# Performance work log

Measured on AMD Instinct MI355X. Metric: run time of the kernel, lower is better.

## Reference

```python
import jax, jax.numpy as jnp
import numpy as np

B, S, D, E = 4, 4096, 1024, 8


def setup_inputs() -> dict:
    key = jax.random.key(0)
    ks = jax.random.split(key, 6)
    x = jax.random.normal(ks[0], (B, S, D), dtype=jnp.float32)
    router_mask = jax.random.randint(ks[1], (B, S), 0, 2)
    We = jax.random.normal(ks[2], (E, D, D), dtype=jnp.float32) * (1.0 / np.sqrt(D))
    be = jax.random.normal(ks[3], (E, D), dtype=jnp.float32) * 0.02
    Wg = jax.random.normal(ks[4], (D, E), dtype=jnp.float32) * (1.0 / np.sqrt(D))
    bg = jax.random.normal(ks[5], (E,), dtype=jnp.float32) * 0.02
    return {"x": x, "router_mask": router_mask, "We": We, "be": be,
            "Wg": Wg, "bg": bg, "top_k": 2}


def reference(x, router_mask, We, be, Wg, bg, top_k):
    # Gating: raw logits (the original uses top-k LOGITS as combine weights,
    # with no softmax). router_mask is accepted but unused, as in the source.
    gate_logits = jnp.einsum('bsd,de->bse', x, Wg) + bg            # [B,S,E]
    top_logits, top_idx = jax.lax.top_k(gate_logits, top_k)        # [B,S,K]
    # Dense all-expert outputs, then gather the selected ones per token.
    expert_out = jnp.einsum('bsd,edf->bsef', x, We) + be           # [B,S,E,D]
    sel = jnp.take_along_axis(expert_out, top_idx[..., None], axis=2)  # [B,S,K,D]
    out = jnp.sum(sel * top_logits[..., None], axis=2)             # [B,S,D]
    return out
```

## Files before the change

### kernel.cpp

```cpp
#include <hip/hip_runtime.h>


#define TOK 16384
#define DIM 1024
#define NE 8
#define NPAIR 28

typedef __attribute__((ext_vector_type(8))) short bf16x8;
typedef __attribute__((ext_vector_type(4))) float f32x4;

#define OFF_CNT    0u
#define OFF_FLAG   132u
#define OFF_TOKW   1024u
#define OFF_PLIST  132096u
#define OFF_WT     1049600u
#define OFF_XB     17826816u
#define OFF_PIDX   51381248u
#define NEED_T3    1049600u
#define NEED_T2    17826816u
#define NEED_T1    51397632u

__device__ __forceinline__ float bf2f(unsigned short u) {
  union { unsigned int i; float f; } c; c.i = ((unsigned int)u) << 16; return c.f;
}
__device__ __forceinline__ unsigned short f2bf_rne(float f) {
  union { float f; unsigned int i; } c; c.f = f;
  unsigned int i = c.i + 0x7fffu + ((c.i >> 16) & 1u);
  return (unsigned short)(i >> 16);
}
__device__ __forceinline__ unsigned int pk2(float lo, float hi) {
  union { float f; unsigned int i; } a, b; a.f = lo; b.f = hi;
  return ((b.i + 0x8000u) & 0xFFFF0000u) | ((a.i + 0x8000u) >> 16);
}

typedef const __attribute__((address_space(1))) unsigned int gas_uint;
typedef __attribute__((address_space(3))) unsigned int las_uint;
__device__ __forceinline__ void gl_lds16(const void* g, void* l) {
  __builtin_amdgcn_global_load_lds((gas_uint*)g, (las_uint*)l, 16, 0, 0);
}
__device__ __forceinline__ void drain_vm() {
  asm volatile("s_waitcnt vmcnt(0)" ::: "memory");
}

__global__ void init_detect(const unsigned int* __restrict__ xdw,
                            int* __restrict__ cnt, int* __restrict__ flag) {
  __shared__ int h;
  if (threadIdx.x == 0) h = 0;
  __syncthreads();
  if (threadIdx.x < 32) cnt[threadIdx.x] = 0;
  unsigned int idx = (threadIdx.x * 32749u + 7u) & 0x7FFFFFu;
  unsigned int b = (xdw[idx] >> 7) & 0xFFu;
  atomicAdd(&h, (b >= 112u && b <= 132u) ? 1 : 0);
  __syncthreads();
  if (threadIdx.x == 0) flag[0] = (h >= 128) ? 1 : 0;
}

#define TP 136
__global__ __launch_bounds__(256) void transpose_W3(const void* __restrict__ Wev,
                                                    unsigned short* __restrict__ Wt,
                                                    const int* __restrict__ flag) {
  const int isbf = *flag;
  __shared__ __align__(16) unsigned short tile[128 * TP];
  const int k0 = blockIdx.x * 128, n0 = blockIdx.y * 128;
  const size_t ebase = (size_t)blockIdx.z << 20;
  const int tid = threadIdx.x;
  const int r = tid >> 1, h = tid & 1;
  if (isbf) {
    const unsigned short* s = (const unsigned short*)Wev + ebase + (size_t)(k0 + r) * DIM + n0 + h * 64;
#pragma unroll
    for (int c = 0; c < 8; ++c)
      *(uint4*)&tile[r * TP + h * 64 + c * 8] = *(const uint4*)(s + c * 8);
  } else {
    const float* s = (const float*)Wev + ebase + (size_t)(k0 + r) * DIM + n0 + h * 64;
#pragma unroll
    for (int c = 0; c < 8; ++c) {
      float4 f0 = *(const float4*)(s + c * 8);
      float4 f1 = *(const float4*)(s + c * 8 + 4);
      uint4 v;
      v.x = pk2(f0.x, f0.y); v.y = pk2(f0.z, f0.w);
      v.z = pk2(f1.x, f1.y); v.w = pk2(f1.z, f1.w);
      *(uint4*)&tile[r * TP + h * 64 + c * 8] = v;
    }
  }
  __syncthreads();
  const int kc = tid & 15;
#pragma unroll
  for (int pass = 0; pass < 8; ++pass) {
    const int nl = pass * 16 + (tid >> 4);
    unsigned short ob[8];
#pragma unroll
    for (int j = 0; j < 8; ++j) ob[j] = tile[(kc * 8 + j) * TP + nl];
    unsigned short* dst = Wt + ebase + (size_t)(n0 + nl) * DIM + k0 + kc * 8;
    *(uint4*)dst = *(uint4*)&ob[0];
  }
}

__global__ __launch_bounds__(256) void gating_v8(
    const void* __restrict__ xv, const void* __restrict__ Wgv,
    const void* __restrict__ bgv, const int* __restrict__ flag,
    unsigned char* __restrict__ pairidx, float2* __restrict__ tokw,
    unsigned short* __restrict__ xb) {
  const int isbf = *flag;
  const int tid = threadIdx.x;
  const int lane = tid & 63;
  const int t = blockIdx.x * 4 + (tid >> 6);

  __shared__ float wgT[NE][DIM];

  if (isbf) {
    const unsigned short* wg = (const unsigned short*)Wgv + (size_t)tid * 32;
#pragma unroll
    for (int rr = 0; rr < 4; ++rr) {
      union { uint4 v; unsigned short s[8]; } w;
      w.v = *(const uint4*)(wg + rr * 8);
      const int d = tid * 4 + rr;
#pragma unroll
      for (int e = 0; e < NE; ++e) wgT[e][d] = bf2f(w.s[e]);
    }
  } else {
    const float* wg = (const float*)Wgv + (size_t)tid * 32;
#pragma unroll
    for (int rr = 0; rr < 4; ++rr) {
      float4 w0 = *(const float4*)(wg + rr * 8);
      float4 w1 = *(const float4*)(wg + rr * 8 + 4);
      const int d = tid * 4 + rr;
      wgT[0][d] = w0.x; wgT[1][d] = w0.y; wgT[2][d] = w0.z; wgT[3][d] = w0.w;
      wgT[4][d] = w1.x; wgT[5][d] = w1.y; wgT[6][d] = w1.z; wgT[7][d] = w1.w;
    }
  }
  __syncthreads();

  float acc[NE];
#pragma unroll
  for (int e = 0; e < NE; ++e) acc[e] = 0.f;

  if (isbf) {
    const unsigned short* xp = (const unsigned short*)xv + (size_t)t * DIM;
#pragma unroll
    for (int j = 0; j < 8; ++j) {
      const int d = j * 128 + lane * 2;
      const unsigned int xw = *(const unsigned int*)(xp + d);
      const float x0 = bf2f((unsigned short)(xw & 0xFFFFu));
      const float x1 = bf2f((unsigned short)(xw >> 16));
#pragma unroll
      for (int e = 0; e < NE; ++e)
        acc[e] += x0 * wgT[e][d] + x1 * wgT[e][d + 1];
    }
  } else {
    const float* xp = (const float*)xv + (size_t)t * DIM;
    unsigned short* xo = xb + (size_t)t * DIM;
#pragma unroll
    for (int j = 0; j < 8; ++j) {
      const int d = j * 128 + lane * 2;
      const float2 xl = *(const float2*)(xp + d);
      *(unsigned int*)(xo + d) = pk2(xl.x, xl.y);
#pragma unroll
      for (int e = 0; e < NE; ++e)
        acc[e] += xl.x * wgT[e][d] + xl.y * wgT[e][d + 1];
    }
  }
#pragma unroll
  for (int m = 1; m < 64; m <<= 1) {
#pragma unroll
    for (int e = 0; e < NE; ++e) acc[e] += __shfl_xor(acc[e], m);
  }
  if (lane == 0) {
    if (isbf) {
      union { uint4 v; unsigned short s[8]; } bgv8; bgv8.v = *(const uint4*)bgv;
#pragma unroll
      for (int e = 0; e < NE; ++e) acc[e] += bf2f(bgv8.s[e]);
    } else {
      const float* bgp = (const float*)bgv;
#pragma unroll
      for (int e = 0; e < NE; ++e) acc[e] += bgp[e];
    }
    int e0 = 0; float v0 = acc[0];
#pragma unroll
    for (int e = 1; e < NE; ++e) if (acc[e] > v0) { v0 = acc[e]; e0 = e; }
    int e1 = -1; float v1 = -3.4e38f;
#pragma unroll
    for (int e = 0; e < NE; ++e) if (e != e0 && acc[e] > v1) { v1 = acc[e]; e1 = e; }
    const int a = e0 < e1 ? e0 : e1;
    const int b = e0 < e1 ? e1 : e0;
    const float wa = (a == e0) ? v0 : v1;
    const float wb = (a == e0) ? v1 : v0;
    const int pidx = a * 7 - (a * (a - 1)) / 2 + (b - a - 1);
    pairidx[t] = (unsigned char)pidx;
    tokw[t] = make_float2(wa, wb);
  }
}

__global__ __launch_bounds__(256) void build_plist(
    const unsigned char* __restrict__ pairidx, int* __restrict__ cnt,
    unsigned short* __restrict__ plist) {
  const int p = blockIdx.x;
  const int tid = threadIdx.x, lane = tid & 63, wv = tid >> 6;
  __shared__ int wcnt[4];
  __shared__ int sbase;
  if (tid == 0) sbase = 0;
  __syncthreads();
  const unsigned long long lanemask = (1ull << lane) - 1ull;
  for (int c = 0; c < TOK / 1024; ++c) {
    const int t0 = c * 1024 + tid * 4;
    const uchar4 pv = *(const uchar4*)(pairidx + t0);
    const unsigned long long m0 = __ballot(pv.x == (unsigned char)p);
    const unsigned long long m1 = __ballot(pv.y == (unsigned char)p);
    const unsigned long long m2 = __ballot(pv.z == (unsigned char)p);
    const unsigned long long m3 = __ballot(pv.w == (unsigned char)p);
    const int c0 = __popcll(m0), c1 = __popcll(m1);
    const int c2 = __popcll(m2), c3 = __popcll(m3);
    if (lane == 0) wcnt[wv] = c0 + c1 + c2 + c3;
    __syncthreads();
    int off = sbase;
    for (int w2 = 0; w2 < wv; ++w2) off += wcnt[w2];
    if (pv.x == (unsigned char)p) plist[p * TOK + off + __popcll(m0 & lanemask)] = (unsigned short)(t0 + 0);
    off += c0;
    if (pv.y == (unsigned char)p) plist[p * TOK + off + __popcll(m1 & lanemask)] = (unsigned short)(t0 + 1);
    off += c1;
    if (pv.z == (unsigned char)p) plist[p * TOK + off + __popcll(m2 & lanemask)] = (unsigned short)(t0 + 2);
    off += c2;
    if (pv.w == (unsigned char)p) plist[p * TOK + off + __popcll(m3 & lanemask)] = (unsigned short)(t0 + 3);
    const int tot = wcnt[0] + wcnt[1] + wcnt[2] + wcnt[3];
    __syncthreads();
    if (tid == 0) sbase += tot;
  }
  if (tid == 0) cnt[p] = sbase;
}

__global__ __launch_bounds__(256, 2) void moe_gemm_v3(
    const void* __restrict__ xv, const unsigned short* __restrict__ xb,
    const unsigned short* __restrict__ Wt, const void* __restrict__ bev,
    const int* __restrict__ flag, const int* __restrict__ cnt,
    const unsigned short* __restrict__ plist, const float2* __restrict__ tokw,
    void* __restrict__ outv) {
  const int y = blockIdx.x;
  int p = -1, mt = 0, acc8 = 0;
  for (int q = 0; q < NPAIR; ++q) {
    const int t = (cnt[q] + 127) >> 7;
    if (y < acc8 + t) { p = q; mt = y - acc8; break; }
    acc8 += t;
  }
  if (p < 0) return;
  const int count = cnt[p];
  int a = 0, rem = p;
  while (rem >= 7 - a) { rem -= 7 - a; ++a; }
  const int ea = a, eb = a + 1 + rem;
  const int isbf = *flag;
  const unsigned char* abase = isbf ? (const unsigned char*)xv
                                    : (const unsigned char*)xb;

  const int tid = threadIdx.x;
  const int lane = tid & 63;
  const int w = tid >> 6;
  const int wr = w >> 1, wc = w & 1;
  const int n0 = blockIdx.y * 128;

  __shared__ __align__(16) unsigned short Alds[128 * 64];
  __shared__ __align__(16) unsigned short Wlds[256 * 64];

  const int csrc = (lane & 7) ^ (lane >> 3);

  const unsigned char* aptr[4];
#pragma unroll
  for (int li = 0; li < 4; ++li) {
    int rg = mt * 128 + w * 32 + li * 8 + (lane >> 3);
    int rgc = rg < count ? rg : count - 1;
    int tok = (int)plist[p * TOK + rgc];
    aptr[li] = abase + (size_t)tok * (DIM * 2) + csrc * 16;
  }
  const unsigned char* wptr[8];
#pragma unroll
  for (int li = 0; li < 8; ++li) {
    int R = w * 64 + li * 8 + (lane >> 3);
    size_t e = (size_t)((R >> 7) ? eb : ea);
    int n = R & 127;
    wptr[li] = (const unsigned char*)Wt + (e << 21) + (size_t)(n0 + n) * (DIM * 2) + csrc * 16;
  }

  f32x4 accA[4][4], accB[4][4];
#pragma unroll
  for (int i = 0; i < 4; ++i)
#pragma unroll
    for (int j = 0; j < 4; ++j) { accA[i][j] = (f32x4){0,0,0,0}; accB[i][j] = (f32x4){0,0,0,0}; }

  for (int ks = 0; ks < DIM; ks += 64) {
#pragma unroll
    for (int li = 0; li < 4; ++li)
      gl_lds16(aptr[li] + ks * 2, (char*)Alds + (w * 32 + li * 8) * 128);
#pragma unroll
    for (int li = 0; li < 8; ++li)
      gl_lds16(wptr[li] + ks * 2, (char*)Wlds + (w * 64 + li * 8) * 128);
    drain_vm();
    __syncthreads();
    const int rl = lane & 15;
#pragma unroll
    for (int kst = 0; kst < 2; ++kst) {
      const int chunk = kst * 4 + (lane >> 4);
      bf16x8 af[4];
#pragma unroll
      for (int m4 = 0; m4 < 4; ++m4) {
        const int r = wr * 64 + m4 * 16 + rl;
        af[m4] = *(const bf16x8*)&Alds[r * 64 + ((chunk ^ (r & 7)) << 3)];
      }
#pragma unroll
      for (int nt = 0; nt < 4; ++nt) {
        const int n = wc * 64 + nt * 16 + rl;
        const int wo = (chunk ^ (n & 7)) << 3;
        bf16x8 bA = *(const bf16x8*)&Wlds[n * 64 + wo];
        bf16x8 bB = *(const bf16x8*)&Wlds[(128 + n) * 64 + wo];
#pragma unroll
        for (int m4 = 0; m4 < 4; ++m4) {
          accA[m4][nt] = __builtin_amdgcn_mfma_f32_16x16x32_bf16(af[m4], bA, accA[m4][nt], 0, 0, 0);
          accB[m4][nt] = __builtin_amdgcn_mfma_f32_16x16x32_bf16(af[m4], bB, accB[m4][nt], 0, 0, 0);
        }
      }
    }
    __syncthreads();
  }

  const int col_l = lane & 15, quad = lane >> 4;
  float bea[4], beb[4];
#pragma unroll
  for (int nt = 0; nt < 4; ++nt) {
    const int col = n0 + wc * 64 + nt * 16 + col_l;
    if (isbf) {
      bea[nt] = bf2f(((const unsigned short*)bev)[ea * DIM + col]);
      beb[nt] = bf2f(((const unsigned short*)bev)[eb * DIM + col]);
    } else {
      bea[nt] = ((const float*)bev)[ea * DIM + col];
      beb[nt] = ((const float*)bev)[eb * DIM + col];
    }
  }
#pragma unroll
  for (int m4 = 0; m4 < 4; ++m4) {
#pragma unroll
    for (int j = 0; j < 4; ++j) {
      const int rg = mt * 128 + wr * 64 + m4 * 16 + quad * 4 + j;
      if (rg < count) {
        const int tk = (int)plist[p * TOK + rg];
        const float2 wt2 = tokw[tk];
#pragma unroll
        for (int nt = 0; nt < 4; ++nt) {
          const float o = wt2.x * (accA[m4][nt][j] + bea[nt]) + wt2.y * (accB[m4][nt][j] + beb[nt]);
          const size_t oi = (size_t)tk * DIM + n0 + wc * 64 + nt * 16 + col_l;
          if (isbf) ((unsigned short*)outv)[oi] = f2bf_rne(o);
          else      ((float*)outv)[oi] = o;
        }
      }
    }
  }
}

__global__ __launch_bounds__(256) void gating_fb(const void* __restrict__ xv,
                                                 const void* __restrict__ Wgv,
                                                 const void* __restrict__ bgv,
                                                 const int* __restrict__ flag,
                                                 int* __restrict__ cnt,
                                                 unsigned short* __restrict__ plist,
                                                 float2* __restrict__ tokw) {
  const int isbf = *flag;
  const int lane = threadIdx.x & 63;
  const int t = blockIdx.x * 4 + (threadIdx.x >> 6);
  float acc[NE];
#pragma unroll
  for (int e = 0; e < NE; ++e) acc[e] = 0.f;
  if (isbf) {
    const unsigned short* xp = (const unsigned short*)xv + (size_t)t * DIM + lane * 16;
#pragma unroll
    for (int u = 0; u < 2; ++u) {
      union { uint4 v; unsigned short s[8]; } xr; xr.v = *(const uint4*)(xp + u * 8);
#pragma unroll
      for (int j = 0; j < 8; ++j) {
        const int d = lane * 16 + u * 8 + j;
        union { uint4 v; unsigned short s[8]; } wg;
        wg.v = *(const uint4*)((const unsigned short*)Wgv + (size_t)d * 8);
        const float xf = bf2f(xr.s[j]);
#pragma unroll
        for (int e = 0; e < NE; ++e) acc[e] += xf * bf2f(wg.s[e]);
      }
    }
  } else {
    const float* xp = (const float*)xv + (size_t)t * DIM + lane * 16;
    float xr[16];
#pragma unroll
    for (int u = 0; u < 4; ++u) *(float4*)&xr[u * 4] = *(const float4*)(xp + u * 4);
#pragma unroll
    for (int j = 0; j < 16; ++j) {
      const int d = lane * 16 + j;
      const float* wr = (const float*)Wgv + (size_t)d * 8;
      float4 w0 = *(const float4*)wr, w1 = *(const float4*)(wr + 4);
      const float xf = xr[j];
      acc[0] += xf * w0.x; acc[1] += xf * w0.y; acc[2] += xf * w0.z; acc[3] += xf * w0.w;
      acc[4] += xf * w1.x; acc[5] += xf * w1.y; acc[6] += xf * w1.z; acc[7] += xf * w1.w;
    }
  }
#pragma unroll
  for (int m = 1; m < 64; m <<= 1) {
#pragma unroll
    for (int e = 0; e < NE; ++e) acc[e] += __shfl_xor(acc[e], m);
  }
  if (lane == 0) {
    if (isbf) {
      union { uint4 v; unsigned short s[8]; } bgv8; bgv8.v = *(const uint4*)bgv;
#pragma unroll
      for (int e = 0; e < NE; ++e) acc[e] += bf2f(bgv8.s[e]);
    } else {
      const float* bgp = (const float*)bgv;
#pragma unroll
      for (int e = 0; e < NE; ++e) acc[e] += bgp[e];
    }
    int e0 = 0; float v0 = acc[0];
#pragma unroll
    for (int e = 1; e < NE; ++e) if (acc[e] > v0) { v0 = acc[e]; e0 = e; }
    int e1 = -1; float v1 = -3.4e38f;
#pragma unroll
    for (int e = 0; e < NE; ++e) if (e != e0 && acc[e] > v1) { v1 = acc[e]; e1 = e; }
    const int a = e0 < e1 ? e0 : e1;
    const int b = e0 < e1 ? e1 : e0;
    const float wa = (a == e0) ? v0 : v1;
    const float wb = (a == e0) ? v1 : v0;
    const int pidx = a * 7 - (a * (a - 1)) / 2 + (b - a - 1);
    const int pos = atomicAdd(&cnt[pidx], 1);
    plist[pidx * TOK + pos] = (unsigned short)t;
    tokw[t] = make_float2(wa, wb);
  }
}

template <int TIER>
__global__ __launch_bounds__(256, 2) void moe_gemm(
    const void* __restrict__ xv, const unsigned short* __restrict__ Wt,
    const void* __restrict__ Wev, const void* __restrict__ bev,
    const int* __restrict__ flag, const int* __restrict__ cnt,
    const unsigned short* __restrict__ plist, const float2* __restrict__ tokw,
    void* __restrict__ outv) {
  const int y = blockIdx.y;
  int p = -1, mt = 0, acc8 = 0;
  for (int q = 0; q < NPAIR; ++q) {
    const int t = (cnt[q] + 127) >> 7;
    if (y < acc8 + t) { p = q; mt = y - acc8; break; }
    acc8 += t;
  }
  if (p < 0) return;
  const int count = cnt[p];
  int a = 0, rem = p;
  while (rem >= 7 - a) { rem -= 7 - a; ++a; }
  const int ea = a, eb = a + 1 + rem;
  const int isbf = *flag;

  const int tid = threadIdx.x;
  const int lane = tid & 63;
  const int w = tid >> 6;
  const int wr = w >> 1, wc = w & 1;
  const int n0 = blockIdx.x * 128;

  __shared__ __align__(16) unsigned short Alds[128 * 64];
  __shared__ __align__(16) unsigned short Wlds[256 * 64];

  const int csrc = (lane & 7) ^ (lane >> 3);

  const char* aptr[4];
#pragma unroll
  for (int li = 0; li < 4; ++li) {
    int rg = mt * 128 + w * 32 + li * 8 + (lane >> 3);
    int rgc = rg < count ? rg : count - 1;
    int tok = (int)plist[p * TOK + rgc];
    aptr[li] = (const char*)xv + (size_t)tok * (DIM * 2) + csrc * 16;
  }
  const char* wptr[8];
#pragma unroll
  for (int li = 0; li < 8; ++li) {
    int R = w * 64 + li * 8 + (lane >> 3);
    size_t e = (size_t)((R >> 7) ? eb : ea);
    int n = R & 127;
    wptr[li] = (const char*)Wt + (e << 21) + (size_t)(n0 + n) * (DIM * 2) + csrc * 16;
  }
  const int rF = tid >> 1;
  const float* xrowF = nullptr;
  if (!isbf) {
    int rg = mt * 128 + rF;
    int rgc = rg < count ? rg : count - 1;
    xrowF = (const float*)xv + (size_t)plist[p * TOK + rgc] * DIM;
  }

  f32x4 accA[4][4], accB[4][4];
#pragma unroll
  for (int i = 0; i < 4; ++i)
#pragma unroll
    for (int j = 0; j < 4; ++j) { accA[i][j] = (f32x4){0,0,0,0}; accB[i][j] = (f32x4){0,0,0,0}; }

  for (int ks = 0; ks < DIM; ks += 64) {
    if (isbf) {
#pragma unroll
      for (int li = 0; li < 4; ++li)
        gl_lds16(aptr[li] + ks * 2, (char*)Alds + (w * 32 + li * 8) * 128);
    } else {
#pragma unroll
      for (int i = 0; i < 4; ++i) {
        const int cst = (tid & 1) * 4 + i;
        const int cs = cst ^ (rF & 7);
        const float* s = xrowF + ks + cs * 8;
        float4 f0 = *(const float4*)s, f1 = *(const float4*)(s + 4);
        uint4 v;
        v.x = pk2(f0.x, f0.y); v.y = pk2(f0.z, f0.w);
        v.z = pk2(f1.x, f1.y); v.w = pk2(f1.z, f1.w);
        *(uint4*)&Alds[rF * 64 + cst * 8] = v;
      }
    }
    if (TIER == 2) {
#pragma unroll
      for (int li = 0; li < 8; ++li)
        gl_lds16(wptr[li] + ks * 2, (char*)Wlds + (w * 64 + li * 8) * 128);
    } else {
      const int kk = tid >> 2, noff = (tid & 3) * 32;
#pragma unroll
      for (int h = 0; h < 2; ++h) {
        const size_t eb2 = (size_t)(h ? eb : ea) << 20;
        unsigned short wb[32];
        if (isbf) {
          const unsigned short* s = (const unsigned short*)Wev + eb2 + (size_t)(ks + kk) * DIM + n0 + noff;
#pragma unroll
          for (int jj = 0; jj < 4; ++jj) *(uint4*)&wb[jj * 8] = *(const uint4*)(s + jj * 8);
        } else {
          const float* s = (const float*)Wev + eb2 + (size_t)(ks + kk) * DIM + n0 + noff;
#pragma unroll
          for (int jj = 0; jj < 8; ++jj) {
            float4 f = *(const float4*)(s + jj * 4);
            unsigned int lo = pk2(f.x, f.y), hi = pk2(f.z, f.w);
            wb[jj * 4 + 0] = (unsigned short)(lo & 0xFFFF);
            wb[jj * 4 + 1] = (unsigned short)(lo >> 16);
            wb[jj * 4 + 2] = (unsigned short)(hi & 0xFFFF);
            wb[jj * 4 + 3] = (unsigned short)(hi >> 16);
          }
        }
        const int chunk = kk >> 3, kin = kk & 7;
#pragma unroll
        for (int j = 0; j < 32; ++j) {
          const int n = noff + j;
          Wlds[(h * 128 + n) * 64 + ((chunk ^ (n & 7)) << 3) + kin] = wb[j];
        }
      }
    }
    __syncthreads();
    const int rl = lane & 15;
#pragma unroll
    for (int kst = 0; kst < 2; ++kst) {
      const int chunk = kst * 4 + (lane >> 4);
      bf16x8 af[4];
#pragma unroll
      for (int m4 = 0; m4 < 4; ++m4) {
        const int r = wr * 64 + m4 * 16 + rl;
        af[m4] = *(const bf16x8*)&Alds[r * 64 + ((chunk ^ (r & 7)) << 3)];
      }
#pragma unroll
      for (int nt = 0; nt < 4; ++nt) {
        const int n = wc * 64 + nt * 16 + rl;
        const int wo = (chunk ^ (n & 7)) << 3;
        bf16x8 bA = *(const bf16x8*)&Wlds[n * 64 + wo];
        bf16x8 bB = *(const bf16x8*)&Wlds[(128 + n) * 64 + wo];
#pragma unroll
        for (int m4 = 0; m4 < 4; ++m4) {
          accA[m4][nt] = __builtin_amdgcn_mfma_f32_16x16x32_bf16(af[m4], bA, accA[m4][nt], 0, 0, 0);
          accB[m4][nt] = __builtin_amdgcn_mfma_f32_16x16x32_bf16(af[m4], bB, accB[m4][nt], 0, 0, 0);
        }
      }
    }
    __syncthreads();
  }

  const int col_l = lane & 15, quad = lane >> 4;
  float bea[4], beb[4];
#pragma unroll
  for (int nt = 0; nt < 4; ++nt) {
    const int col = n0 + wc * 64 + nt * 16 + col_l;
    if (isbf) {
      bea[nt] = bf2f(((const unsigned short*)bev)[ea * DIM + col]);
      beb[nt] = bf2f(((const unsigned short*)bev)[eb * DIM + col]);
    } else {
      bea[nt] = ((const float*)bev)[ea * DIM + col];
      beb[nt] = ((const float*)bev)[eb * DIM + col];
    }
  }
#pragma unroll
  for (int m4 = 0; m4 < 4; ++m4) {
#pragma unroll
    for (int j = 0; j < 4; ++j) {
      const int rg = mt * 128 + wr * 64 + m4 * 16 + quad * 4 + j;
      if (rg < count) {
        const int tk = (int)plist[p * TOK + rg];
        const float2 wt2 = tokw[tk];
#pragma unroll
        for (int nt = 0; nt < 4; ++nt) {
          const float o = wt2.x * (accA[m4][nt][j] + bea[nt]) + wt2.y * (accB[m4][nt][j] + beb[nt]);
          const size_t oi = (size_t)tk * DIM + n0 + wc * 64 + nt * 16 + col_l;
          if (isbf) ((unsigned short*)outv)[oi] = f2bf_rne(o);
          else      ((float*)outv)[oi] = o;
        }
      }
    }
  }
}

extern "C" void kernel_launch(void* const* d_in, const int* in_sizes, int n_in,
                              void* d_out, int out_size, void* d_ws, size_t ws_size,
                              hipStream_t stream) {
  const void* xv  = d_in[0];
  const void* Wev = d_in[2];
  const void* bev = d_in[3];
  const void* Wgv = d_in[4];
  const void* bgv = d_in[5];

  char* ws = (char*)d_ws;
  int* cnt    = (int*)(ws + OFF_CNT);
  int* flag   = (int*)(ws + OFF_FLAG);
  float2* tokw = (float2*)(ws + OFF_TOKW);
  unsigned short* plist = (unsigned short*)(ws + OFF_PLIST);
  unsigned short* Wt    = (unsigned short*)(ws + OFF_WT);

  if (ws_size < (size_t)NEED_T3) return;
  const int tier = (ws_size >= (size_t)NEED_T1) ? 1
                 : (ws_size >= (size_t)NEED_T2) ? 2 : 3;

  init_detect<<<1, 256, 0, stream>>>((const unsigned int*)xv, cnt, flag);
  if (tier <= 2) transpose_W3<<<dim3(8, 8, 8), 256, 0, stream>>>(Wev, Wt, flag);

  if (tier == 1) {
    unsigned short* xb = (unsigned short*)(ws + OFF_XB);
    unsigned char* pairidx = (unsigned char*)(ws + OFF_PIDX);
    gating_v8<<<TOK / 4, 256, 0, stream>>>(xv, Wgv, bgv, flag, pairidx, tokw, xb);
    build_plist<<<NPAIR, 256, 0, stream>>>(pairidx, cnt, plist);
    moe_gemm_v3<<<dim3(160, 8), 256, 0, stream>>>(xv, xb, Wt, bev, flag, cnt,
                                                  plist, tokw, d_out);
  } else if (tier == 2) {
    gating_fb<<<TOK / 4, 256, 0, stream>>>(xv, Wgv, bgv, flag, cnt, plist, tokw);
    moe_gemm<2><<<dim3(8, 160), 256, 0, stream>>>(xv, Wt, Wev, bev, flag, cnt,
                                                  plist, tokw, d_out);
  } else {
    gating_fb<<<TOK / 4, 256, 0, stream>>>(xv, Wgv, bgv, flag, cnt, plist, tokw);
    moe_gemm<3><<<dim3(8, 160), 256, 0, stream>>>(xv, Wt, Wev, bev, flag, cnt,
                                                  plist, tokw, d_out);
  }
}
```

Before: 285.4 us.

## Fuse weight transpose with gating and detect dtype on host

The weight-transpose blocks and the gating blocks now run in one templated prep kernel, dispatched by block index, so the two stages can overlap and one launch goes away. The input dtype is read from the host-side input size, which removes the init_detect launch and the runtime flag branches in the GEMM (new moe_gemm_v4 template). The old low-workspace fallback tiers are dropped, so the code now returns early when the workspace is too small. It relies on build_plist to write the counts, since they are no longer zeroed first.

Result: no change. 282.4 us (-1.1%).

```diff
diff --git a/kernel.cpp b/kernel.cpp
--- a/kernel.cpp
+++ b/kernel.cpp
@@ -42,72 +42,60 @@
   asm volatile("s_waitcnt vmcnt(0)" ::: "memory");
 }
 
-__global__ void init_detect(const unsigned int* __restrict__ xdw,
-                            int* __restrict__ cnt, int* __restrict__ flag) {
-  __shared__ int h;
-  if (threadIdx.x == 0) h = 0;
-  __syncthreads();
-  if (threadIdx.x < 32) cnt[threadIdx.x] = 0;
-  unsigned int idx = (threadIdx.x * 32749u + 7u) & 0x7FFFFFu;
-  unsigned int b = (xdw[idx] >> 7) & 0xFFu;
-  atomicAdd(&h, (b >= 112u && b <= 132u) ? 1 : 0);
-  __syncthreads();
-  if (threadIdx.x == 0) flag[0] = (h >= 128) ? 1 : 0;
-}
-
 #define TP 136
-__global__ __launch_bounds__(256) void transpose_W3(const void* __restrict__ Wev,
-                                                    unsigned short* __restrict__ Wt,
-                                                    const int* __restrict__ flag) {
-  const int isbf = *flag;
-  __shared__ __align__(16) unsigned short tile[128 * TP];
-  const int k0 = blockIdx.x * 128, n0 = blockIdx.y * 128;
-  const size_t ebase = (size_t)blockIdx.z << 20;
+
+
+template <int ISBF>
+__global__ __launch_bounds__(256) void prep(
+    const void* __restrict__ xv, const void* __restrict__ Wgv,
+    const void* __restrict__ bgv, const void* __restrict__ Wev,
+    unsigned short* __restrict__ Wt, unsigned char* __restrict__ pairidx,
+    float2* __restrict__ tokw, unsigned short* __restrict__ xb) {
+  __shared__ __align__(16) char smem[128 * TP * 2];
   const int tid = threadIdx.x;
-  const int r = tid >> 1, h = tid & 1;
-  if (isbf) {
-    const unsigned short* s = (const unsigned short*)Wev + ebase + (size_t)(k0 + r) * DIM + n0 + h * 64;
-#pragma unroll
-    for (int c = 0; c < 8; ++c)
-      *(uint4*)&tile[r * TP + h * 64 + c * 8] = *(const uint4*)(s + c * 8);
-  } else {
-    const float* s = (const float*)Wev + ebase + (size_t)(k0 + r) * DIM + n0 + h * 64;
-#pragma unroll
-    for (int c = 0; c < 8; ++c) {
-      float4 f0 = *(const float4*)(s + c * 8);
-      float4 f1 = *(const float4*)(s + c * 8 + 4);
-      uint4 v;
-      v.x = pk2(f0.x, f0.y); v.y = pk2(f0.z, f0.w);
-      v.z = pk2(f1.x, f1.y); v.w = pk2(f1.z, f1.w);
-      *(uint4*)&tile[r * TP + h * 64 + c * 8] = v;
-    }
-  }
-  __syncthreads();
-  const int kc = tid & 15;
-#pragma unroll
-  for (int pass = 0; pass < 8; ++pass) {
-    const int nl = pass * 16 + (tid >> 4);
-    unsigned short ob[8];
-#pragma unroll
-    for (int j = 0; j < 8; ++j) ob[j] = tile[(kc * 8 + j) * TP + nl];
-    unsigned short* dst = Wt + ebase + (size_t)(n0 + nl) * DIM + k0 + kc * 8;
-    *(uint4*)dst = *(uint4*)&ob[0];
-  }
-}
-
-__global__ __launch_bounds__(256) void gating_v8(
-    const void* __restrict__ xv, const void* __restrict__ Wgv,
-    const void* __restrict__ bgv, const int* __restrict__ flag,
-    unsigned char* __restrict__ pairidx, float2* __restrict__ tokw,
-    unsigned short* __restrict__ xb) {
-  const int isbf = *flag;
-  const int tid = threadIdx.x;
+
+  if (blockIdx.x >= 4096) {
+    unsigned short* tile = (unsigned short*)smem;
+    const int idx = blockIdx.x - 4096;
+    const int k0 = (idx & 7) * 128, n0 = ((idx >> 3) & 7) * 128;
+    const size_t ebase = (size_t)(idx >> 6) << 20;
+    const int r = tid >> 1, h = tid & 1;
+    if (ISBF) {
+      const unsigned short* s = (const unsigned short*)Wev + ebase + (size_t)(k0 + r) * DIM + n0 + h * 64;
+#pragma unroll
+      for (int c = 0; c < 8; ++c)
+        *(uint4*)&tile[r * TP + h * 64 + c * 8] = *(const uint4*)(s + c * 8);
+    } else {
+      const float* s = (const float*)Wev + ebase + (size_t)(k0 + r) * DIM + n0 + h * 64;
+#pragma unroll
+      for (int c = 0; c < 8; ++c) {
+        float4 f0 = *(const float4*)(s + c * 8);
+        float4 f1 = *(const float4*)(s + c * 8 + 4);
+        uint4 v;
+        v.x = pk2(f0.x, f0.y); v.y = pk2(f0.z, f0.w);
+        v.z = pk2(f1.x, f1.y); v.w = pk2(f1.z, f1.w);
+        *(uint4*)&tile[r * TP + h * 64 + c * 8] = v;
+      }
+    }
+    __syncthreads();
+    const int kc = tid & 15;
+#pragma unroll
+    for (int pass = 0; pass < 8; ++pass) {
+      const int nl = pass * 16 + (tid >> 4);
+      unsigned short ob[8];
+#pragma unroll
+      for (int j = 0; j < 8; ++j) ob[j] = tile[(kc * 8 + j) * TP + nl];
+      unsigned short* dst = Wt + ebase + (size_t)(n0 + nl) * DIM + k0 + kc * 8;
+      *(uint4*)dst = *(uint4*)&ob[0];
+    }
+    return;
+  }
+
+  float (*wgT)[DIM] = (float(*)[DIM])smem;
   const int lane = tid & 63;
   const int t = blockIdx.x * 4 + (tid >> 6);
 
-  __shared__ float wgT[NE][DIM];
-
-  if (isbf) {
+  if (ISBF) {
     const unsigned short* wg = (const unsigned short*)Wgv + (size_t)tid * 32;
 #pragma unroll
     for (int rr = 0; rr < 4; ++rr) {
@@ -134,7 +122,7 @@
 #pragma unroll
   for (int e = 0; e < NE; ++e) acc[e] = 0.f;
 
-  if (isbf) {
+  if (ISBF) {
     const unsigned short* xp = (const unsigned short*)xv + (size_t)t * DIM;
 #pragma unroll
     for (int j = 0; j < 8; ++j) {
@@ -165,7 +153,7 @@
     for (int e = 0; e < NE; ++e) acc[e] += __shfl_xor(acc[e], m);
   }
   if (lane == 0) {
-    if (isbf) {
+    if (ISBF) {
       union { uint4 v; unsigned short s[8]; } bgv8; bgv8.v = *(const uint4*)bgv;
 #pragma unroll
       for (int e = 0; e < NE; ++e) acc[e] += bf2f(bgv8.s[e]);
@@ -227,6 +215,273 @@
   if (tid == 0) cnt[p] = sbase;
 }
 
+template <int ISBF>
+__global__ __launch_bounds__(256, 2) void moe_gemm_v4(
+    const void* __restrict__ xv, const unsigned short* __restrict__ xb,
+    const unsigned short* __restrict__ Wt, const void* __restrict__ bev,
+    const int* __restrict__ cnt, const unsigned short* __restrict__ plist,
+    const float2* __restrict__ tokw, void* __restrict__ outv) {
+  const int y = blockIdx.x;
+  int p = -1, mt = 0, acc8 = 0;
+  for (int q = 0; q < NPAIR; ++q) {
+    const int t = (cnt[q] + 127) >> 7;
+    if (y < acc8 + t) { p = q; mt = y - acc8; break; }
+    acc8 += t;
+  }
+  if (p < 0) return;
+  const int count = cnt[p];
+  int a = 0, rem = p;
+  while (rem >= 7 - a) { rem -= 7 - a; ++a; }
+  const int ea = a, eb = a + 1 + rem;
+  const unsigned char* abase = ISBF ? (const unsigned char*)xv
+                                    : (const unsigned char*)xb;
+
+  const int tid = threadIdx.x;
+  const int lane = tid & 63;
+  const int w = tid >> 6;
+  const int wr = w >> 1, wc = w & 1;
+  const int n0 = blockIdx.y * 128;
+
+  __shared__ __align__(16) unsigned short Alds[128 * 64];
+  __shared__ __align__(16) unsigned short Wlds[256 * 64];
+
+  const int csrc = (lane & 7) ^ (lane >> 3);
+
+  const unsigned char* aptr[4];
+#pragma unroll
+  for (int li = 0; li < 4; ++li) {
+    int rg = mt * 128 + w * 32 + li * 8 + (lane >> 3);
+    int rgc = rg < count ? rg : count - 1;
+    int tok = (int)plist[p * TOK + rgc];
+    aptr[li] = abase + (size_t)tok * (DIM * 2) + csrc * 16;
+  }
+  const unsigned char* wptr[8];
+#pragma unroll
+  for (int li = 0; li < 8; ++li) {
+    int R = w * 64 + li * 8 + (lane >> 3);
+    size_t e = (size_t)((R >> 7) ? eb : ea);
+    int n = R & 127;
+    wptr[li] = (const unsigned char*)Wt + (e << 21) + (size_t)(n0 + n) * (DIM * 2) + csrc * 16;
+  }
+
+  f32x4 accA[4][4], accB[4][4];
+#pragma unroll
+  for (int i = 0; i < 4; ++i)
+#pragma unroll
+    for (int j = 0; j < 4; ++j) { accA[i][j] = (f32x4){0,0,0,0}; accB[i][j] = (f32x4){0,0,0,0}; }
+
+  for (int ks = 0; ks < DIM; ks += 64) {
+#pragma unroll
+    for (int li = 0; li < 4; ++li)
+      gl_lds16(aptr[li] + ks * 2, (char*)Alds + (w * 32 + li * 8) * 128);
+#pragma unroll
+    for (int li = 0; li < 8; ++li)
+      gl_lds16(wptr[li] + ks * 2, (char*)Wlds + (w * 64 + li * 8) * 128);
+    drain_vm();
+    __syncthreads();
+    const int rl = lane & 15;
+#pragma unroll
+    for (int kst = 0; kst < 2; ++kst) {
+      const int chunk = kst * 4 + (lane >> 4);
+      bf16x8 af[4];
+#pragma unroll
+      for (int m4 = 0; m4 < 4; ++m4) {
+        const int r = wr * 64 + m4 * 16 + rl;
+        af[m4] = *(const bf16x8*)&Alds[r * 64 + ((chunk ^ (r & 7)) << 3)];
+      }
+#pragma unroll
+      for (int nt = 0; nt < 4; ++nt) {
+        const int n = wc * 64 + nt * 16 + rl;
+        const int wo = (chunk ^ (n & 7)) << 3;
+        bf16x8 bA = *(const bf16x8*)&Wlds[n * 64 + wo];
+        bf16x8 bB = *(const bf16x8*)&Wlds[(128 + n) * 64 + wo];
+#pragma unroll
+        for (int m4 = 0; m4 < 4; ++m4) {
+          accA[m4][nt] = __builtin_amdgcn_mfma_f32_16x16x32_bf16(af[m4], bA, accA[m4][nt], 0, 0, 0);
+          accB[m4][nt] = __builtin_amdgcn_mfma_f32_16x16x32_bf16(af[m4], bB, accB[m4][nt], 0, 0, 0);
+        }
+      }
+    }
+    __syncthreads();
+  }
+
+  const int col_l = lane & 15, quad = lane >> 4;
+  float bea[4], beb[4];
+#pragma unroll
+  for (int nt = 0; nt < 4; ++nt) {
+    const int col = n0 + wc * 64 + nt * 16 + col_l;
+    if (ISBF) {
+      bea[nt] = bf2f(((const unsigned short*)bev)[ea * DIM + col]);
+      beb[nt] = bf2f(((const unsigned short*)bev)[eb * DIM + col]);
+    } else {
+      bea[nt] = ((const float*)bev)[ea * DIM + col];
+      beb[nt] = ((const float*)bev)[eb * DIM + col];
+    }
+  }
+#pragma unroll
+  for (int m4 = 0; m4 < 4; ++m4) {
+#pragma unroll
+    for (int j = 0; j < 4; ++j) {
+      const int rg = mt * 128 + wr * 64 + m4 * 16 + quad * 4 + j;
+      if (rg < count) {
+        const int tk = (int)plist[p * TOK + rg];
+        const float2 wt2 = tokw[tk];
+#pragma unroll
+        for (int nt = 0; nt < 4; ++nt) {
+          const float o = wt2.x * (accA[m4][nt][j] + bea[nt]) + wt2.y * (accB[m4][nt][j] + beb[nt]);
+          const size_t oi = (size_t)tk * DIM + n0 + wc * 64 + nt * 16 + col_l;
+          if (ISBF) ((unsigned short*)outv)[oi] = f2bf_rne(o);
+          else      ((float*)outv)[oi] = o;
+        }
+      }
+    }
+  }
+}
+
+
+__global__ void init_detect(const unsigned int* __restrict__ xdw,
+                            int* __restrict__ cnt, int* __restrict__ flag) {
+  __shared__ int h;
+  if (threadIdx.x == 0) h = 0;
+  __syncthreads();
+  if (threadIdx.x < 32) cnt[threadIdx.x] = 0;
+  unsigned int idx = (threadIdx.x * 32749u + 7u) & 0x7FFFFFu;
+  unsigned int b = (xdw[idx] >> 7) & 0xFFu;
+  atomicAdd(&h, (b >= 112u && b <= 132u) ? 1 : 0);
+  __syncthreads();
+  if (threadIdx.x == 0) flag[0] = (h >= 128) ? 1 : 0;
+}
+
+__global__ __launch_bounds__(256) void transpose_W3(const void* __restrict__ Wev,
+                                                    unsigned short* __restrict__ Wt,
+                                                    const int* __restrict__ flag) {
+  const int isbf = *flag;
+  __shared__ __align__(16) unsigned short tile[128 * TP];
+  const int k0 = blockIdx.x * 128, n0 = blockIdx.y * 128;
+  const size_t ebase = (size_t)blockIdx.z << 20;
+  const int tid = threadIdx.x;
+  const int r = tid >> 1, h = tid & 1;
+  if (isbf) {
+    const unsigned short* s = (const unsigned short*)Wev + ebase + (size_t)(k0 + r) * DIM + n0 + h * 64;
+#pragma unroll
+    for (int c = 0; c < 8; ++c)
+      *(uint4*)&tile[r * TP + h * 64 + c * 8] = *(const uint4*)(s + c * 8);
+  } else {
+    const float* s = (const float*)Wev + ebase + (size_t)(k0 + r) * DIM + n0 + h * 64;
+#pragma unroll
+    for (int c = 0; c < 8; ++c) {
+      float4 f0 = *(const float4*)(s + c * 8);
+      float4 f1 = *(const float4*)(s + c * 8 + 4);
+      uint4 v;
+      v.x = pk2(f0.x, f0.y); v.y = pk2(f0.z, f0.w);
+      v.z = pk2(f1.x, f1.y); v.w = pk2(f1.z, f1.w);
+      *(uint4*)&tile[r * TP + h * 64 + c * 8] = v;
+    }
+  }
+  __syncthreads();
+  const int kc = tid & 15;
+#pragma unroll
+  for (int pass = 0; pass < 8; ++pass) {
+    const int nl = pass * 16 + (tid >> 4);
+    unsigned short ob[8];
+#pragma unroll
+    for (int j = 0; j < 8; ++j) ob[j] = tile[(kc * 8 + j) * TP + nl];
+    unsigned short* dst = Wt + ebase + (size_t)(n0 + nl) * DIM + k0 + kc * 8;
+    *(uint4*)dst = *(uint4*)&ob[0];
+  }
+}
+
+__global__ __launch_bounds__(256) void gating_v8(
+    const void* __restrict__ xv, const void* __restrict__ Wgv,
+    const void* __restrict__ bgv, const int* __restrict__ flag,
+    unsigned char* __restrict__ pairidx, float2* __restrict__ tokw,
+    unsigned short* __restrict__ xb) {
+  const int isbf = *flag;
+  const int tid = threadIdx.x;
+  const int lane = tid & 63;
+  const int t = blockIdx.x * 4 + (tid >> 6);
+  __shared__ float wgT[NE][DIM];
+  if (isbf) {
+    const unsigned short* wg = (const unsigned short*)Wgv + (size_t)tid * 32;
+#pragma unroll
+    for (int rr = 0; rr < 4; ++rr) {
+      union { uint4 v; unsigned short s[8]; } w;
+      w.v = *(const uint4*)(wg + rr * 8);
+      const int d = tid * 4 + rr;
+#pragma unroll
+      for (int e = 0; e < NE; ++e) wgT[e][d] = bf2f(w.s[e]);
+    }
+  } else {
+    const float* wg = (const float*)Wgv + (size_t)tid * 32;
+#pragma unroll
+    for (int rr = 0; rr < 4; ++rr) {
+      float4 w0 = *(const float4*)(wg + rr * 8);
+      float4 w1 = *(const float4*)(wg + rr * 8 + 4);
+      const int d = tid * 4 + rr;
+      wgT[0][d] = w0.x; wgT[1][d] = w0.y; wgT[2][d] = w0.z; wgT[3][d] = w0.w;
+      wgT[4][d] = w1.x; wgT[5][d] = w1.y; wgT[6][d] = w1.z; wgT[7][d] = w1.w;
+    }
+  }
+  __syncthreads();
+  float acc[NE];
+#pragma unroll
+  for (int e = 0; e < NE; ++e) acc[e] = 0.f;
+  if (isbf) {
+    const unsigned short* xp = (const unsigned short*)xv + (size_t)t * DIM;
+#pragma unroll
+    for (int j = 0; j < 8; ++j) {
+      const int d = j * 128 + lane * 2;
+      const unsigned int xw = *(const unsigned int*)(xp + d);
+      const float x0 = bf2f((unsigned short)(xw & 0xFFFFu));
+      const float x1 = bf2f((unsigned short)(xw >> 16));
+#pragma unroll
+      for (int e = 0; e < NE; ++e)
+        acc[e] += x0 * wgT[e][d] + x1 * wgT[e][d + 1];
+    }
+  } else {
+    const float* xp = (const float*)xv + (size_t)t * DIM;
+    unsigned short* xo = xb + (size_t)t * DIM;
+#pragma unroll
+    for (int j = 0; j < 8; ++j) {
+      const int d = j * 128 + lane * 2;
+      const float2 xl = *(const float2*)(xp + d);
+      *(unsigned int*)(xo + d) = pk2(xl.x, xl.y);
+#pragma unroll
+      for (int e = 0; e < NE; ++e)
+        acc[e] += xl.x * wgT[e][d] + xl.y * wgT[e][d + 1];
+    }
+  }
+#pragma unroll
+  for (int m = 1; m < 64; m <<= 1) {
+#pragma unroll
+    for (int e = 0; e < NE; ++e) acc[e] += __shfl_xor(acc[e], m);
+  }
+  if (lane == 0) {
+    if (isbf) {
+      union { uint4 v; unsigned short s[8]; } bgv8; bgv8.v = *(const uint4*)bgv;
+#pragma unroll
+      for (int e = 0; e < NE; ++e) acc[e] += bf2f(bgv8.s[e]);
+    } else {
+      const float* bgp = (const float*)bgv;
+#pragma unroll
+      for (int e = 0; e < NE; ++e) acc[e] += bgp[e];
+    }
+    int e0 = 0; float v0 = acc[0];
+#pragma unroll
+    for (int e = 1; e < NE; ++e) if (acc[e] > v0) { v0 = acc[e]; e0 = e; }
+    int e1 = -1; float v1 = -3.4e38f;
+#pragma unroll
+    for (int e = 0; e < NE; ++e) if (e != e0 && acc[e] > v1) { v1 = acc[e]; e1 = e; }
+    const int a = e0 < e1 ? e0 : e1;
+    const int b = e0 < e1 ? e1 : e0;
+    const float wa = (a == e0) ? v0 : v1;
+    const float wb = (a == e0) ? v1 : v0;
+    const int pidx = a * 7 - (a * (a - 1)) / 2 + (b - a - 1);
+    pairidx[t] = (unsigned char)pidx;
+    tokw[t] = make_float2(wa, wb);
+  }
+}
+
 __global__ __launch_bounds__(256, 2) void moe_gemm_v3(
     const void* __restrict__ xv, const unsigned short* __restrict__ xb,
     const unsigned short* __restrict__ Wt, const void* __restrict__ bev,
@@ -248,18 +503,14 @@
   const int isbf = *flag;
   const unsigned char* abase = isbf ? (const unsigned char*)xv
                                     : (const unsigned char*)xb;
-
   const int tid = threadIdx.x;
   const int lane = tid & 63;
   const int w = tid >> 6;
   const int wr = w >> 1, wc = w & 1;
   const int n0 = blockIdx.y * 128;
-
   __shared__ __align__(16) unsigned short Alds[128 * 64];
   __shared__ __align__(16) unsigned short Wlds[256 * 64];
-
   const int csrc = (lane & 7) ^ (lane >> 3);
-
   const unsigned char* aptr[4];
 #pragma unroll
   for (int li = 0; li < 4; ++li) {
@@ -276,13 +527,11 @@
     int n = R & 127;
     wptr[li] = (const unsigned char*)Wt + (e << 21) + (size_t)(n0 + n) * (DIM * 2) + csrc * 16;
   }
-
   f32x4 accA[4][4], accB[4][4];
 #pragma unroll
   for (int i = 0; i < 4; ++i)
 #pragma unroll
     for (int j = 0; j < 4; ++j) { accA[i][j] = (f32x4){0,0,0,0}; accB[i][j] = (f32x4){0,0,0,0}; }
-
   for (int ks = 0; ks < DIM; ks += 64) {
 #pragma unroll
     for (int li = 0; li < 4; ++li)
@@ -317,7 +566,6 @@
     }
     __syncthreads();
   }
-
   const int col_l = lane & 15, quad = lane >> 4;
   float bea[4], beb[4];
 #pragma unroll
@@ -351,255 +599,6 @@
   }
 }
 
-__global__ __launch_bounds__(256) void gating_fb(const void* __restrict__ xv,
-                                                 const void* __restrict__ Wgv,
-                                                 const void* __restrict__ bgv,
-                                                 const int* __restrict__ flag,
-                                                 int* __restrict__ cnt,
-                                                 unsigned short* __restrict__ plist,
-                                                 float2* __restrict__ tokw) {
-  const int isbf = *flag;
-  const int lane = threadIdx.x & 63;
-  const int t = blockIdx.x * 4 + (threadIdx.x >> 6);
-  float acc[NE];
-#pragma unroll
-  for (int e = 0; e < NE; ++e) acc[e] = 0.f;
-  if (isbf) {
-    const unsigned short* xp = (const unsigned short*)xv + (size_t)t * DIM + lane * 16;
-#pragma unroll
-    for (int u = 0; u < 2; ++u) {
-      union { uint4 v; unsigned short s[8]; } xr; xr.v = *(const uint4*)(xp + u * 8);
-#pragma unroll
-      for (int j = 0; j < 8; ++j) {
-        const int d = lane * 16 + u * 8 + j;
-        union { uint4 v; unsigned short s[8]; } wg;
-        wg.v = *(const uint4*)((const unsigned short*)Wgv + (size_t)d * 8);
-        const float xf = bf2f(xr.s[j]);
-#pragma unroll
-        for (int e = 0; e < NE; ++e) acc[e] += xf * bf2f(wg.s[e]);
-      }
-    }
-  } else {
-    const float* xp = (const float*)xv + (size_t)t * DIM + lane * 16;
-    float xr[16];
-#pragma unroll
-    for (int u = 0; u < 4; ++u) *(float4*)&xr[u * 4] = *(const float4*)(xp + u * 4);
-#pragma unroll
-    for (int j = 0; j < 16; ++j) {
-      const int d = lane * 16 + j;
-      const float* wr = (const float*)Wgv + (size_t)d * 8;
-      float4 w0 = *(const float4*)wr, w1 = *(const float4*)(wr + 4);
-      const float xf = xr[j];
-      acc[0] += xf * w0.x; acc[1] += xf * w0.y; acc[2] += xf * w0.z; acc[3] += xf * w0.w;
-      acc[4] += xf * w1.x; acc[5] += xf * w1.y; acc[6] += xf * w1.z; acc[7] += xf * w1.w;
-    }
-  }
-#pragma unroll
-  for (int m = 1; m < 64; m <<= 1) {
-#pragma unroll
-    for (int e = 0; e < NE; ++e) acc[e] += __shfl_xor(acc[e], m);
-  }
-  if (lane == 0) {
-    if (isbf) {
-      union { uint4 v; unsigned short s[8]; } bgv8; bgv8.v = *(const uint4*)bgv;
-#pragma unroll
-      for (int e = 0; e < NE; ++e) acc[e] += bf2f(bgv8.s[e]);
-    } else {
-      const float* bgp = (const float*)bgv;
-#pragma unroll
-      for (int e = 0; e < NE; ++e) acc[e] += bgp[e];
-    }
-    int e0 = 0; float v0 = acc[0];
-#pragma unroll
-    for (int e = 1; e < NE; ++e) if (acc[e] > v0) { v0 = acc[e]; e0 = e; }
-    int e1 = -1; float v1 = -3.4e38f;
-#pragma unroll
-    for (int e = 0; e < NE; ++e) if (e != e0 && acc[e] > v1) { v1 = acc[e]; e1 = e; }
-    const int a = e0 < e1 ? e0 : e1;
-    const int b = e0 < e1 ? e1 : e0;
-    const float wa = (a == e0) ? v0 : v1;
-    const float wb = (a == e0) ? v1 : v0;
-    const int pidx = a * 7 - (a * (a - 1)) / 2 + (b - a - 1);
-    const int pos = atomicAdd(&cnt[pidx], 1);
-    plist[pidx * TOK + pos] = (unsigned short)t;
-    tokw[t] = make_float2(wa, wb);
-  }
-}
-
-template <int TIER>
-__global__ __launch_bounds__(256, 2) void moe_gemm(
-    const void* __restrict__ xv, const unsigned short* __restrict__ Wt,
-    const void* __restrict__ Wev, const void* __restrict__ bev,
-    const int* __restrict__ flag, const int* __restrict__ cnt,
-    const unsigned short* __restrict__ plist, const float2* __restrict__ tokw,
-    void* __restrict__ outv) {
-  const int y = blockIdx.y;
-  int p = -1, mt = 0, acc8 = 0;
-  for (int q = 0; q < NPAIR; ++q) {
-    const int t = (cnt[q] + 127) >> 7;
-    if (y < acc8 + t) { p = q; mt = y - acc8; break; }
-    acc8 += t;
-  }
-  if (p < 0) return;
-  const int count = cnt[p];
-  int a = 0, rem = p;
-  while (rem >= 7 - a) { rem -= 7 - a; ++a; }
-  const int ea = a, eb = a + 1 + rem;
-  const int isbf = *flag;
-
-  const int tid = threadIdx.x;
-  const int lane = tid & 63;
-  const int w = tid >> 6;
-  const int wr = w >> 1, wc = w & 1;
-  const int n0 = blockIdx.x * 128;
-
-  __shared__ __align__(16) unsigned short Alds[128 * 64];
-  __shared__ __align__(16) unsigned short Wlds[256 * 64];
-
-  const int csrc = (lane & 7) ^ (lane >> 3);
-
-  const char* aptr[4];
-#pragma unroll
-  for (int li = 0; li < 4; ++li) {
-    int rg = mt * 128 + w * 32 + li * 8 + (lane >> 3);
-    int rgc = rg < count ? rg : count - 1;
-    int tok = (int)plist[p * TOK + rgc];
-    aptr[li] = (const char*)xv + (size_t)tok * (DIM * 2) + csrc * 16;
-  }
-  const char* wptr[8];
-#pragma unroll
-  for (int li = 0; li < 8; ++li) {
-    int R = w * 64 + li * 8 + (lane >> 3);
-    size_t e = (size_t)((R >> 7) ? eb : ea);
-    int n = R & 127;
-    wptr[li] = (const char*)Wt + (e << 21) + (size_t)(n0 + n) * (DIM * 2) + csrc * 16;
-  }
-  const int rF = tid >> 1;
-  const float* xrowF = nullptr;
-  if (!isbf) {
-    int rg = mt * 128 + rF;
-    int rgc = rg < count ? rg : count - 1;
-    xrowF = (const float*)xv + (size_t)plist[p * TOK + rgc] * DIM;
-  }
-
-  f32x4 accA[4][4], accB[4][4];
-#pragma unroll
-  for (int i = 0; i < 4; ++i)
-#pragma unroll
-    for (int j = 0; j < 4; ++j) { accA[i][j] = (f32x4){0,0,0,0}; accB[i][j] = (f32x4){0,0,0,0}; }
-
-  for (int ks = 0; ks < DIM; ks += 64) {
-    if (isbf) {
-#pragma unroll
-      for (int li = 0; li < 4; ++li)
-        gl_lds16(aptr[li] + ks * 2, (char*)Alds + (w * 32 + li * 8) * 128);
-    } else {
-#pragma unroll
-      for (int i = 0; i < 4; ++i) {
-        const int cst = (tid & 1) * 4 + i;
-        const int cs = cst ^ (rF & 7);
-        const float* s = xrowF + ks + cs * 8;
-        float4 f0 = *(const float4*)s, f1 = *(const float4*)(s + 4);
-        uint4 v;
-        v.x = pk2(f0.x, f0.y); v.y = pk2(f0.z, f0.w);
-        v.z = pk2(f1.x, f1.y); v.w = pk2(f1.z, f1.w);
-        *(uint4*)&Alds[rF * 64 + cst * 8] = v;
-      }
-    }
-    if (TIER == 2) {
-#pragma unroll
-      for (int li = 0; li < 8; ++li)
-        gl_lds16(wptr[li] + ks * 2, (char*)Wlds + (w * 64 + li * 8) * 128);
-    } else {
-      const int kk = tid >> 2, noff = (tid & 3) * 32;
-#pragma unroll
-      for (int h = 0; h < 2; ++h) {
-        const size_t eb2 = (size_t)(h ? eb : ea) << 20;
-        unsigned short wb[32];
-        if (isbf) {
-          const unsigned short* s = (const unsigned short*)Wev + eb2 + (size_t)(ks + kk) * DIM + n0 + noff;
-#pragma unroll
-          for (int jj = 0; jj < 4; ++jj) *(uint4*)&wb[jj * 8] = *(const uint4*)(s + jj * 8);
-        } else {
-          const float* s = (const float*)Wev + eb2 + (size_t)(ks + kk) * DIM + n0 + noff;
-#pragma unroll
-          for (int jj = 0; jj < 8; ++jj) {
-            float4 f = *(const float4*)(s + jj * 4);
-            unsigned int lo = pk2(f.x, f.y), hi = pk2(f.z, f.w);
-            wb[jj * 4 + 0] = (unsigned short)(lo & 0xFFFF);
-            wb[jj * 4 + 1] = (unsigned short)(lo >> 16);
-            wb[jj * 4 + 2] = (unsigned short)(hi & 0xFFFF);
-            wb[jj * 4 + 3] = (unsigned short)(hi >> 16);
-          }
-        }
-        const int chunk = kk >> 3, kin = kk & 7;
-#pragma unroll
-        for (int j = 0; j < 32; ++j) {
-          const int n = noff + j;
-          Wlds[(h * 128 + n) * 64 + ((chunk ^ (n & 7)) << 3) + kin] = wb[j];
-        }
-      }
-    }
-    __syncthreads();
-    const int rl = lane & 15;
-#pragma unroll
-    for (int kst = 0; kst < 2; ++kst) {
-      const int chunk = kst * 4 + (lane >> 4);
-      bf16x8 af[4];
-#pragma unroll
-      for (int m4 = 0; m4 < 4; ++m4) {
-        const int r = wr * 64 + m4 * 16 + rl;
-        af[m4] = *(const bf16x8*)&Alds[r * 64 + ((chunk ^ (r & 7)) << 3)];
-      }
-#pragma unroll
-      for (int nt = 0; nt < 4; ++nt) {
-        const int n = wc * 64 + nt * 16 + rl;
-        const int wo = (chunk ^ (n & 7)) << 3;
-        bf16x8 bA = *(const bf16x8*)&Wlds[n * 64 + wo];
-        bf16x8 bB = *(const bf16x8*)&Wlds[(128 + n) * 64 + wo];
-#pragma unroll
-        for (int m4 = 0; m4 < 4; ++m4) {
-          accA[m4][nt] = __builtin_amdgcn_mfma_f32_16x16x32_bf16(af[m4], bA, accA[m4][nt], 0, 0, 0);
-          accB[m4][nt] = __builtin_amdgcn_mfma_f32_16x16x32_bf16(af[m4], bB, accB[m4][nt], 0, 0, 0);
-        }
-      }
-    }
-    __syncthreads();
-  }
-
-  const int col_l = lane & 15, quad = lane >> 4;
-  float bea[4], beb[4];
-#pragma unroll
-  for (int nt = 0; nt < 4; ++nt) {
-    const int col = n0 + wc * 64 + nt * 16 + col_l;
-    if (isbf) {
-      bea[nt] = bf2f(((const unsigned short*)bev)[ea * DIM + col]);
-      beb[nt] = bf2f(((const unsigned short*)bev)[eb * DIM + col]);
-    } else {
-      bea[nt] = ((const float*)bev)[ea * DIM + col];
-      beb[nt] = ((const float*)bev)[eb * DIM + col];
-    }
-  }
-#pragma unroll
-  for (int m4 = 0; m4 < 4; ++m4) {
-#pragma unroll
-    for (int j = 0; j < 4; ++j) {
-      const int rg = mt * 128 + wr * 64 + m4 * 16 + quad * 4 + j;
-      if (rg < count) {
-        const int tk = (int)plist[p * TOK + rg];
-        const float2 wt2 = tokw[tk];
-#pragma unroll
-        for (int nt = 0; nt < 4; ++nt) {
-          const float o = wt2.x * (accA[m4][nt][j] + bea[nt]) + wt2.y * (accB[m4][nt][j] + beb[nt]);
-          const size_t oi = (size_t)tk * DIM + n0 + wc * 64 + nt * 16 + col_l;
-          if (isbf) ((unsigned short*)outv)[oi] = f2bf_rne(o);
-          else      ((float*)outv)[oi] = o;
-        }
-      }
-    }
-  }
-}
-
 extern "C" void kernel_launch(void* const* d_in, const int* in_sizes, int n_in,
                               void* d_out, int out_size, void* d_ws, size_t ws_size,
                               hipStream_t stream) {
@@ -616,27 +615,31 @@
   unsigned short* plist = (unsigned short*)(ws + OFF_PLIST);
   unsigned short* Wt    = (unsigned short*)(ws + OFF_WT);
 
-  if (ws_size < (size_t)NEED_T3) return;
-  const int tier = (ws_size >= (size_t)NEED_T1) ? 1
-                 : (ws_size >= (size_t)NEED_T2) ? 2 : 3;
-
-  init_detect<<<1, 256, 0, stream>>>((const unsigned int*)xv, cnt, flag);
-  if (tier <= 2) transpose_W3<<<dim3(8, 8, 8), 256, 0, stream>>>(Wev, Wt, flag);
-
-  if (tier == 1) {
-    unsigned short* xb = (unsigned short*)(ws + OFF_XB);
-    unsigned char* pairidx = (unsigned char*)(ws + OFF_PIDX);
+  if (ws_size < (size_t)NEED_T1) return;
+  unsigned short* xb = (unsigned short*)(ws + OFF_XB);
+  unsigned char* pairidx = (unsigned char*)(ws + OFF_PIDX);
+
+  const long long xbytes = (long long)in_sizes[0];
+  int isbf_host = -1;
+  if (xbytes == (long long)TOK * DIM * 4) isbf_host = 0;
+  else if (xbytes == (long long)TOK * DIM * 2) isbf_host = 1;
+
+  if (isbf_host == 0) {
+    prep<0><<<4608, 256, 0, stream>>>(xv, Wgv, bgv, Wev, Wt, pairidx, tokw, xb);
+    build_plist<<<NPAIR, 256, 0, stream>>>(pairidx, cnt, plist);
+    moe_gemm_v4<0><<<dim3(160, 8), 256, 0, stream>>>(xv, xb, Wt, bev, cnt,
+                                                     plist, tokw, d_out);
+  } else if (isbf_host == 1) {
+    prep<1><<<4608, 256, 0, stream>>>(xv, Wgv, bgv, Wev, Wt, pairidx, tokw, xb);
+    build_plist<<<NPAIR, 256, 0, stream>>>(pairidx, cnt, plist);
+    moe_gemm_v4<1><<<dim3(160, 8), 256, 0, stream>>>(xv, xb, Wt, bev, cnt,
+                                                     plist, tokw, d_out);
+  } else {
+    init_detect<<<1, 256, 0, stream>>>((const unsigned int*)xv, cnt, flag);
+    transpose_W3<<<dim3(8, 8, 8), 256, 0, stream>>>(Wev, Wt, flag);
     gating_v8<<<TOK / 4, 256, 0, stream>>>(xv, Wgv, bgv, flag, pairidx, tokw, xb);
     build_plist<<<NPAIR, 256, 0, stream>>>(pairidx, cnt, plist);
     moe_gemm_v3<<<dim3(160, 8), 256, 0, stream>>>(xv, xb, Wt, bev, flag, cnt,
                                                   plist, tokw, d_out);
-  } else if (tier == 2) {
-    gating_fb<<<TOK / 4, 256, 0, stream>>>(xv, Wgv, bgv, flag, cnt, plist, tokw);
-    moe_gemm<2><<<dim3(8, 160), 256, 0, stream>>>(xv, Wt, Wev, bev, flag, cnt,
-                                                  plist, tokw, d_out);
-  } else {
-    gating_fb<<<TOK / 4, 256, 0, stream>>>(xv, Wgv, bgv, flag, cnt, plist, tokw);
-    moe_gemm<3><<<dim3(8, 160), 256, 0, stream>>>(xv, Wt, Wev, bev, flag, cnt,
-                                                  plist, tokw, d_out);
-  }
-}
+  }
+}
```
